# Kernel tuning notes

Measured on AMD Instinct MI355X. Metric: run time of the kernel, lower is better.

## Reference

```python
import jax, jax.numpy as jnp
import numpy as np
import math

K_SLOTS = 64
DIM = 512
HEADS = 8
HEAD_DIM = DIM // HEADS
EPS = 1e-20
LN_EPS = 1e-5
SQRT_DIM = 1.0 / math.sqrt(HEAD_DIM)


def layernorm(x, g, b):
    mu = jnp.mean(x, axis=-1, keepdims=True)
    var = jnp.var(x, axis=-1, keepdims=True)
    return (x - mu) * jax.lax.rsqrt(var + LN_EPS) * g + b


def setup_inputs() -> dict:
    key = jax.random.key(0)
    ks = jax.random.split(key, 8)
    B, T = 8, 8192
    lim = 1.0 / math.sqrt(DIM)
    return {
        "X": jax.random.normal(ks[0], (B, T, DIM), jnp.float32),
        "slots_w": jax.random.normal(ks[1], (K_SLOTS, DIM), jnp.float32),
        "g_slots": jnp.ones((DIM,), jnp.float32),
        "b_slots": jnp.zeros((DIM,), jnp.float32),
        "Wk": jax.random.uniform(ks[2], (DIM, DIM), jnp.float32, -lim, lim),
        "bk": jax.random.uniform(ks[3], (DIM,), jnp.float32, -lim, lim),
        "Wv": jax.random.uniform(ks[4], (DIM, DIM), jnp.float32, -lim, lim),
        "bv": jax.random.uniform(ks[5], (DIM,), jnp.float32, -lim, lim),
        "g_after": jnp.ones((DIM,), jnp.float32),
        "b_after": jnp.zeros((DIM,), jnp.float32),
    }


def reference(X, slots_w, g_slots, b_slots, Wk, bk, Wv, bv, g_after, b_after):
    B, T, D = X.shape
    # slots -> queries, shared across batch: (K, D) -> (H, K, hd)
    S = layernorm(slots_w, g_slots, b_slots)
    Q = S.reshape(K_SLOTS, HEADS, HEAD_DIM).transpose(1, 0, 2)  # (H, K, hd)
    # key/value projections, head split: (B, T, D) -> (B, H, T, hd)
    Kx = (X @ Wk.T + bk).reshape(B, T, HEADS, HEAD_DIM).transpose(0, 2, 1, 3)
    V = (X @ Wv.T + bv).reshape(B, T, HEADS, HEAD_DIM).transpose(0, 2, 1, 3)
    # attention logits (B, H, K, T), scale = 1/sqrt(head_dim)
    A = jnp.einsum("hkd,bhsd->bhks", Q, Kx) * SQRT_DIM
    # softmax over the SLOT axis (k), then renormalize by row-sum over s
    W = jax.nn.softmax(A, axis=-2)
    C = jnp.sum(W, axis=-1, keepdims=True)  # (B, H, K, 1)
    A = W / (C + EPS)
    S_hat = jnp.einsum("bhks,bhsd->bhkd", A, V)  # (B, H, K, hd)
    S_hat = S_hat.transpose(0, 2, 1, 3).reshape(B, K_SLOTS, D)
    return layernorm(S_hat, g_after, b_after)
```

## Files before the change

kernel.cpp:

```cpp
#include <hip/hip_runtime.h>
#include <hip/hip_bf16.h>
#include <math.h>

typedef unsigned short ushort_t;
typedef unsigned int u32;

constexpr int D  = 512;
constexpr int T  = 8192;
constexpr int B  = 8;
constexpr int H  = 8;
constexpr int KS = 64;
constexpr int HD = 64;
constexpr float SCALE = 0.125f;
constexpr float LNEPS = 1e-5f;
constexpr float EPS   = 1e-20f;

constexpr int TC  = 128;
constexpr int CPB = 2;

constexpr size_t OFF_S    = 0;
constexpr size_t OFF_BQ   = 32768;
constexpr size_t OFF_SACC = 33280;
constexpr size_t OFF_CACC = 295424;
constexpr size_t OFF_WB2  = 299520;

typedef __attribute__((ext_vector_type(8))) short bf16x8;
typedef __attribute__((ext_vector_type(4))) float f32x4;
typedef __attribute__((ext_vector_type(4))) unsigned short us4;

typedef const __attribute__((address_space(1))) u32* gas_ptr;
typedef __attribute__((address_space(3))) u32* las_ptr;

__device__ __forceinline__ void gload16(const void* g, void* l) {
  __builtin_amdgcn_global_load_lds((gas_ptr)g, (las_ptr)l, 16, 0, 0);
}

__device__ __forceinline__ ushort_t f2bf(float x) {
  __hip_bfloat16 t = __float2bfloat16(x);
  return *(ushort_t*)&t;
}

__device__ __forceinline__ u32 pk2bf(float x, float y) {
  __hip_bfloat162 t = __float22bfloat162_rn(make_float2(x, y));
  return *(u32*)&t;
}

__device__ __forceinline__ bf16x8 cvt8(f32x4 a, f32x4 b) {
  union { bf16x8 v; u32 u[4]; } r;
  r.u[0] = pk2bf(a.x, a.y); r.u[1] = pk2bf(a.z, a.w);
  r.u[2] = pk2bf(b.x, b.y); r.u[3] = pk2bf(b.z, b.w);
  return r.v;
}

__global__ void ln_slots_kernel(const float* __restrict__ slots_w,
                                const float* __restrict__ g, const float* __restrict__ b,
                                float* __restrict__ S) {
  __shared__ float red[8];
  int k = blockIdx.x;
  int tid = threadIdx.x;
  float x0 = slots_w[k*D + tid];
  float x1 = slots_w[k*D + tid + 256];
  float s1 = x0 + x1, s2 = x0*x0 + x1*x1;
  for (int off = 32; off; off >>= 1) { s1 += __shfl_xor(s1, off); s2 += __shfl_xor(s2, off); }
  if ((tid & 63) == 0) { red[tid >> 6] = s1; red[4 + (tid >> 6)] = s2; }
  __syncthreads();
  s1 = red[0] + red[1] + red[2] + red[3];
  s2 = red[4] + red[5] + red[6] + red[7];
  float mu = s1 / D;
  float var = s2 / D - mu * mu;
  float rs = rsqrtf(var + LNEPS);
  S[k*D + tid]       = (x0 - mu) * rs * g[tid]       + b[tid];
  S[k*D + tid + 256] = (x1 - mu) * rs * g[tid + 256] + b[tid + 256];
}

__global__ void weff_kernel(const float* __restrict__ S, const float* __restrict__ Wk,
                            ushort_t* __restrict__ Wb2) {
  int gid = blockIdx.x * 256 + threadIdx.x;
  int in = gid & 511;
  int hk = gid >> 9;
  int h = hk >> 6, k = hk & 63;
  const float* srow = S + k*D + h*HD;
  const float* wcol = Wk + (size_t)(h*HD)*D + in;
  float acc = 0.f;
  #pragma unroll 8
  for (int d = 0; d < HD; ++d) acc += srow[d] * wcol[(size_t)d*D];
  Wb2[(size_t)(h*128 + k)*D + in] = f2bf(acc * SCALE);
}

__global__ void bq_kernel(const float* __restrict__ S, const float* __restrict__ bk,
                          float* __restrict__ bq) {
  int hk = blockIdx.x * 256 + threadIdx.x;
  int h = hk >> 6, k = hk & 63;
  float acc = 0.f;
  for (int d = 0; d < HD; ++d) acc += S[k*D + h*HD + d] * bk[h*HD + d];
  bq[hk] = acc * SCALE;
}

__global__ void wvcopy_kernel(const float* __restrict__ Wv, ushort_t* __restrict__ Wb2) {
  int gid = blockIdx.x * 256 + threadIdx.x;
  int in = gid & 511;
  int hd = gid >> 9;
  int h = hd >> 6, d = hd & 63;
  Wb2[(size_t)(h*128 + 64 + d)*D + in] = f2bf(Wv[(size_t)hd*D + in]);
}

__global__ void zero_kernel(float* __restrict__ p, int n) {
  int gid = blockIdx.x * 256 + threadIdx.x;
  if (gid < n) p[gid] = 0.f;
}

__global__ __launch_bounds__(256, 3) void main_kernel(
    const float* __restrict__ X, const ushort_t* __restrict__ Wb2,
    const float* __restrict__ bq, const float* __restrict__ bv,
    float* __restrict__ Sacc, float* __restrict__ Cacc) {
  __shared__ __align__(16) char smem[34816];
  float*    A_lds = (float*)smem;
  ushort_t* B_lds = (ushort_t*)(smem + 16384);
  ushort_t* W_lds = (ushort_t*)smem;
  ushort_t* V_lds = (ushort_t*)(smem + 17408);

  const int tid  = threadIdx.x;
  const int lane = tid & 63, w = tid >> 6;
  const int wm = w & 1, wn = w >> 1;
  const int m16 = lane & 15, q = lane >> 4;

  const int id = blockIdx.x;
  const int h  = (id >> 3) & 7;
  const int cg = (id & 7) | ((id >> 6) << 3);
  const int bh = (cg >> 5) * H + h;

  f32x4 acc2[4] = {};
  float csum[4] = {0.f, 0.f, 0.f, 0.f};

  for (int cc = 0; cc < CPB; ++cc) {
    const float* Xc = X + (size_t)(cg * CPB + cc) * TC * D;
    f32x4 acc[4][4] = {};

    for (int kb = 0; kb < D; kb += 32) {
      __syncthreads();
      #pragma unroll
      for (int m = 0; m < 4; ++m) {
        int li = tid + m * 256;
        int row = li >> 3, c = li & 7;
        gload16(Xc + (size_t)row * D + kb + c * 4, A_lds + (size_t)li * 4);
      }
      #pragma unroll
      for (int m = 0; m < 2; ++m) {
        int li = tid + m * 256;
        int col = li >> 2, c = li & 3;
        gload16(Wb2 + (size_t)(h * 128 + col) * D + kb + c * 8, B_lds + (size_t)li * 8);
      }
      __syncthreads();
      bf16x8 af[4], bf[4];
      #pragma unroll
      for (int i = 0; i < 4; ++i) {
        const f32x4* ap = (const f32x4*)(A_lds + (wm * 64 + i * 16 + m16) * 32 + q * 8);
        af[i] = cvt8(ap[0], ap[1]);
      }
      #pragma unroll
      for (int j = 0; j < 4; ++j)
        bf[j] = *(const bf16x8*)(B_lds + (wn * 64 + j * 16 + m16) * 32 + q * 8);
      #pragma unroll
      for (int i = 0; i < 4; ++i)
        #pragma unroll
        for (int j = 0; j < 4; ++j)
          acc[i][j] = __builtin_amdgcn_mfma_f32_16x16x32_bf16(af[i], bf[j], acc[i][j], 0, 0, 0);
    }
    __syncthreads();

    if (wn == 0) {
      float bqv[4];
      #pragma unroll
      for (int j = 0; j < 4; ++j) bqv[j] = bq[h * KS + j * 16 + m16];
      #pragma unroll
      for (int i = 0; i < 4; ++i) {
        us4 wp[4];
        #pragma unroll
        for (int r = 0; r < 4; ++r) {
          float v0 = acc[i][0][r] + bqv[0];
          float v1 = acc[i][1][r] + bqv[1];
          float v2 = acc[i][2][r] + bqv[2];
          float v3 = acc[i][3][r] + bqv[3];
          float mx = fmaxf(fmaxf(v0, v1), fmaxf(v2, v3));
          mx = fmaxf(mx, __shfl_xor(mx, 1));
          mx = fmaxf(mx, __shfl_xor(mx, 2));
          mx = fmaxf(mx, __shfl_xor(mx, 4));
          mx = fmaxf(mx, __shfl_xor(mx, 8));
          v0 = __expf(v0 - mx); v1 = __expf(v1 - mx);
          v2 = __expf(v2 - mx); v3 = __expf(v3 - mx);
          float s = v0 + v1 + v2 + v3;
          s += __shfl_xor(s, 1); s += __shfl_xor(s, 2);
          s += __shfl_xor(s, 4); s += __shfl_xor(s, 8);
          float inv = __builtin_amdgcn_rcpf(s);
          v0 *= inv; v1 *= inv; v2 *= inv; v3 *= inv;
          csum[0] += v0; csum[1] += v1; csum[2] += v2; csum[3] += v3;
          wp[0][r] = f2bf(v0); wp[1][r] = f2bf(v1);
          wp[2][r] = f2bf(v2); wp[3][r] = f2bf(v3);
        }
        #pragma unroll
        for (int j = 0; j < 4; ++j)
          *(us4*)(W_lds + (j * 16 + m16) * 136 + wm * 64 + i * 16 + q * 4) = wp[j];
      }
    } else {
      float bvv[4];
      #pragma unroll
      for (int j = 0; j < 4; ++j) bvv[j] = bv[h * HD + j * 16 + m16];
      #pragma unroll
      for (int i = 0; i < 4; ++i) {
        #pragma unroll
        for (int j = 0; j < 4; ++j) {
          us4 pk;
          pk.x = f2bf(acc[i][j][0] + bvv[j]);
          pk.y = f2bf(acc[i][j][1] + bvv[j]);
          pk.z = f2bf(acc[i][j][2] + bvv[j]);
          pk.w = f2bf(acc[i][j][3] + bvv[j]);
          *(us4*)(V_lds + (j * 16 + m16) * 136 + wm * 64 + i * 16 + q * 4) = pk;
        }
      }
    }
    __syncthreads();

    #pragma unroll
    for (int kk = 0; kk < 4; ++kk) {
      bf16x8 a = *(const bf16x8*)(W_lds + (w * 16 + m16) * 136 + kk * 32 + q * 8);
      #pragma unroll
      for (int j = 0; j < 4; ++j) {
        bf16x8 bb = *(const bf16x8*)(V_lds + (j * 16 + m16) * 136 + kk * 32 + q * 8);
        acc2[j] = __builtin_amdgcn_mfma_f32_16x16x32_bf16(a, bb, acc2[j], 0, 0, 0);
      }
    }
  }

  float* Sb = Sacc + (size_t)bh * KS * HD;
  #pragma unroll
  for (int j = 0; j < 4; ++j)
    #pragma unroll
    for (int r = 0; r < 4; ++r)
      atomicAdd(Sb + (w * 16 + q * 4 + r) * HD + j * 16 + m16, acc2[j][r]);

  if (wn == 0) {
    #pragma unroll
    for (int j = 0; j < 4; ++j) {
      float c = csum[j];
      c += __shfl_xor(c, 16);
      c += __shfl_xor(c, 32);
      if (q == 0) atomicAdd(Cacc + (size_t)bh * KS + j * 16 + m16, c);
    }
  }
}

__global__ void finalize_kernel(const float* __restrict__ Sacc, const float* __restrict__ Cacc,
                                const float* __restrict__ g, const float* __restrict__ bb,
                                float* __restrict__ out) {
  __shared__ float red[8];
  int bk_ = blockIdx.x;
  int b = bk_ >> 6, k = bk_ & 63;
  int tid = threadIdx.x;
  float v[2];
  #pragma unroll
  for (int m = 0; m < 2; ++m) {
    int d = tid + m*256;
    int h = d >> 6, dd = d & 63;
    float c = Cacc[((size_t)b*H + h)*KS + k];
    v[m] = Sacc[(((size_t)b*H + h)*KS + k)*HD + dd] / (c + EPS);
  }
  float s1 = v[0] + v[1], s2 = v[0]*v[0] + v[1]*v[1];
  for (int off = 32; off; off >>= 1) { s1 += __shfl_xor(s1, off); s2 += __shfl_xor(s2, off); }
  if ((tid & 63) == 0) { red[tid >> 6] = s1; red[4 + (tid >> 6)] = s2; }
  __syncthreads();
  s1 = red[0] + red[1] + red[2] + red[3];
  s2 = red[4] + red[5] + red[6] + red[7];
  float mu = s1 / D;
  float var = s2 / D - mu * mu;
  float rs = rsqrtf(var + LNEPS);
  #pragma unroll
  for (int m = 0; m < 2; ++m) {
    int d = tid + m*256;
    out[(size_t)bk_*D + d] = (v[m] - mu) * rs * g[d] + bb[d];
  }
}

extern "C" void kernel_launch(void* const* d_in, const int* in_sizes, int n_in,
                              void* d_out, int out_size, void* d_ws, size_t ws_size,
                              hipStream_t stream) {
  const float* X       = (const float*)d_in[0];
  const float* slots_w = (const float*)d_in[1];
  const float* g_slots = (const float*)d_in[2];
  const float* b_slots = (const float*)d_in[3];
  const float* Wk      = (const float*)d_in[4];
  const float* bk      = (const float*)d_in[5];
  const float* Wv      = (const float*)d_in[6];
  const float* bv      = (const float*)d_in[7];
  const float* g_after = (const float*)d_in[8];
  const float* b_after = (const float*)d_in[9];
  float* ws   = (float*)d_ws;
  float* S    = ws + OFF_S;
  float* bq   = ws + OFF_BQ;
  float* Sacc = ws + OFF_SACC;
  float* Cacc = ws + OFF_CACC;
  ushort_t* Wb2 = (ushort_t*)(ws + OFF_WB2);
  float* out  = (float*)d_out;

  hipLaunchKernelGGL(ln_slots_kernel, dim3(64), dim3(256), 0, stream, slots_w, g_slots, b_slots, S);
  hipLaunchKernelGGL(weff_kernel, dim3(1024), dim3(256), 0, stream, S, Wk, Wb2);
  hipLaunchKernelGGL(bq_kernel, dim3(2), dim3(256), 0, stream, S, bk, bq);
  hipLaunchKernelGGL(wvcopy_kernel, dim3(1024), dim3(256), 0, stream, Wv, Wb2);
  hipLaunchKernelGGL(zero_kernel, dim3(1040), dim3(256), 0, stream, Sacc, 266240);
  hipLaunchKernelGGL(main_kernel, dim3(2048), dim3(256), 0, stream, X, Wb2, bq, bv, Sacc, Cacc);
  hipLaunchKernelGGL(finalize_kernel, dim3(B * KS), dim3(256), 0, stream,
                     Sacc, Cacc, g_after, b_after, out);
}
```

Before: 363.0 us.

## Pre-convert X to bf16 and run swizzled-LDS bf16 main kernel

```diff
diff --git a/kernel.cpp b/kernel.cpp
--- a/kernel.cpp
+++ b/kernel.cpp
@@ -23,6 +23,8 @@
 constexpr size_t OFF_SACC = 33280;
 constexpr size_t OFF_CACC = 295424;
 constexpr size_t OFF_WB2  = 299520;
+constexpr size_t OFF_XB   = 561664;
+constexpr size_t WS_NEED  = (OFF_XB + (size_t)B*T*D/2) * 4;
 
 typedef __attribute__((ext_vector_type(8))) short bf16x8;
 typedef __attribute__((ext_vector_type(4))) float f32x4;
@@ -109,13 +111,20 @@
   if (gid < n) p[gid] = 0.f;
 }
 
-__global__ __launch_bounds__(256, 3) void main_kernel(
-    const float* __restrict__ X, const ushort_t* __restrict__ Wb2,
+__global__ void xcvt_kernel(const float* __restrict__ X, ushort_t* __restrict__ Xb) {
+  size_t i = ((size_t)blockIdx.x * 256 + threadIdx.x) * 8;
+  f32x4 a = *(const f32x4*)(X + i);
+  f32x4 b = *(const f32x4*)(X + i + 4);
+  *(bf16x8*)(Xb + i) = cvt8(a, b);
+}
+
+__global__ __launch_bounds__(256, 4) void main_kernel_bf16(
+    const ushort_t* __restrict__ Xb, const ushort_t* __restrict__ Wb2,
     const float* __restrict__ bq, const float* __restrict__ bv,
     float* __restrict__ Sacc, float* __restrict__ Cacc) {
   __shared__ __align__(16) char smem[34816];
-  float*    A_lds = (float*)smem;
-  ushort_t* B_lds = (ushort_t*)(smem + 16384);
+  ushort_t* A_lds = (ushort_t*)smem;
+  ushort_t* B_lds = (ushort_t*)(smem + 8192);
   ushort_t* W_lds = (ushort_t*)smem;
   ushort_t* V_lds = (ushort_t*)(smem + 17408);
 
@@ -123,6 +132,7 @@
   const int lane = tid & 63, w = tid >> 6;
   const int wm = w & 1, wn = w >> 1;
   const int m16 = lane & 15, q = lane >> 4;
+  const int kq = q ^ ((m16 >> 1) & 3);
 
   const int id = blockIdx.x;
   const int h  = (id >> 3) & 7;
@@ -133,38 +143,38 @@
   float csum[4] = {0.f, 0.f, 0.f, 0.f};
 
   for (int cc = 0; cc < CPB; ++cc) {
-    const float* Xc = X + (size_t)(cg * CPB + cc) * TC * D;
+    const ushort_t* Xc = Xb + (size_t)(cg * CPB + cc) * TC * D;
     f32x4 acc[4][4] = {};
 
     for (int kb = 0; kb < D; kb += 32) {
       __syncthreads();
       #pragma unroll
-      for (int m = 0; m < 4; ++m) {
-        int li = tid + m * 256;
-        int row = li >> 3, c = li & 7;
-        gload16(Xc + (size_t)row * D + kb + c * 4, A_lds + (size_t)li * 4);
-      }
-      #pragma unroll
       for (int m = 0; m < 2; ++m) {
         int li = tid + m * 256;
-        int col = li >> 2, c = li & 3;
-        gload16(Wb2 + (size_t)(h * 128 + col) * D + kb + c * 8, B_lds + (size_t)li * 8);
+        int row = li >> 2;
+        int kc = (li & 3) ^ ((row >> 1) & 3);
+        gload16(Xc + (size_t)row * D + kb + kc * 8, A_lds + (size_t)li * 8);
+      }
+      #pragma unroll
+      for (int m = 0; m < 2; ++m) {
+        int li = tid + m * 256;
+        int col = li >> 2;
+        int kc = (li & 3) ^ ((col >> 1) & 3);
+        gload16(Wb2 + (size_t)(h * 128 + col) * D + kb + kc * 8, B_lds + (size_t)li * 8);
       }
       __syncthreads();
-      bf16x8 af[4], bf[4];
-      #pragma unroll
-      for (int i = 0; i < 4; ++i) {
-        const f32x4* ap = (const f32x4*)(A_lds + (wm * 64 + i * 16 + m16) * 32 + q * 8);
-        af[i] = cvt8(ap[0], ap[1]);
-      }
+      bf16x8 af[4], bfv[4];
+      #pragma unroll
+      for (int i = 0; i < 4; ++i)
+        af[i] = *(const bf16x8*)(A_lds + (size_t)(((wm*64 + i*16 + m16) << 2) | kq) * 8);
       #pragma unroll
       for (int j = 0; j < 4; ++j)
-        bf[j] = *(const bf16x8*)(B_lds + (wn * 64 + j * 16 + m16) * 32 + q * 8);
+        bfv[j] = *(const bf16x8*)(B_lds + (size_t)(((wn*64 + j*16 + m16) << 2) | kq) * 8);
       #pragma unroll
       for (int i = 0; i < 4; ++i)
         #pragma unroll
         for (int j = 0; j < 4; ++j)
-          acc[i][j] = __builtin_amdgcn_mfma_f32_16x16x32_bf16(af[i], bf[j], acc[i][j], 0, 0, 0);
+          acc[i][j] = __builtin_amdgcn_mfma_f32_16x16x32_bf16(af[i], bfv[j], acc[i][j], 0, 0, 0);
     }
     __syncthreads();
 
@@ -249,6 +259,145 @@
   }
 }
 
+__global__ __launch_bounds__(256, 3) void main_kernel_f32(
+    const float* __restrict__ X, const ushort_t* __restrict__ Wb2,
+    const float* __restrict__ bq, const float* __restrict__ bv,
+    float* __restrict__ Sacc, float* __restrict__ Cacc) {
+  __shared__ __align__(16) char smem[34816];
+  float*    A_lds = (float*)smem;
+  ushort_t* B_lds = (ushort_t*)(smem + 16384);
+  ushort_t* W_lds = (ushort_t*)smem;
+  ushort_t* V_lds = (ushort_t*)(smem + 17408);
+
+  const int tid  = threadIdx.x;
+  const int lane = tid & 63, w = tid >> 6;
+  const int wm = w & 1, wn = w >> 1;
+  const int m16 = lane & 15, q = lane >> 4;
+
+  const int id = blockIdx.x;
+  const int h  = (id >> 3) & 7;
+  const int cg = (id & 7) | ((id >> 6) << 3);
+  const int bh = (cg >> 5) * H + h;
+
+  f32x4 acc2[4] = {};
+  float csum[4] = {0.f, 0.f, 0.f, 0.f};
+
+  for (int cc = 0; cc < CPB; ++cc) {
+    const float* Xc = X + (size_t)(cg * CPB + cc) * TC * D;
+    f32x4 acc[4][4] = {};
+    for (int kb = 0; kb < D; kb += 32) {
+      __syncthreads();
+      #pragma unroll
+      for (int m = 0; m < 4; ++m) {
+        int li = tid + m * 256;
+        int row = li >> 3, c = li & 7;
+        gload16(Xc + (size_t)row * D + kb + c * 4, A_lds + (size_t)li * 4);
+      }
+      #pragma unroll
+      for (int m = 0; m < 2; ++m) {
+        int li = tid + m * 256;
+        int col = li >> 2, c = li & 3;
+        gload16(Wb2 + (size_t)(h * 128 + col) * D + kb + c * 8, B_lds + (size_t)li * 8);
+      }
+      __syncthreads();
+      bf16x8 af[4], bfv[4];
+      #pragma unroll
+      for (int i = 0; i < 4; ++i) {
+        const f32x4* ap = (const f32x4*)(A_lds + (wm * 64 + i * 16 + m16) * 32 + q * 8);
+        af[i] = cvt8(ap[0], ap[1]);
+      }
+      #pragma unroll
+      for (int j = 0; j < 4; ++j)
+        bfv[j] = *(const bf16x8*)(B_lds + (wn * 64 + j * 16 + m16) * 32 + q * 8);
+      #pragma unroll
+      for (int i = 0; i < 4; ++i)
+        #pragma unroll
+        for (int j = 0; j < 4; ++j)
+          acc[i][j] = __builtin_amdgcn_mfma_f32_16x16x32_bf16(af[i], bfv[j], acc[i][j], 0, 0, 0);
+    }
+    __syncthreads();
+
+    if (wn == 0) {
+      float bqv[4];
+      #pragma unroll
+      for (int j = 0; j < 4; ++j) bqv[j] = bq[h * KS + j * 16 + m16];
+      #pragma unroll
+      for (int i = 0; i < 4; ++i) {
+        us4 wp[4];
+        #pragma unroll
+        for (int r = 0; r < 4; ++r) {
+          float v0 = acc[i][0][r] + bqv[0];
+          float v1 = acc[i][1][r] + bqv[1];
+          float v2 = acc[i][2][r] + bqv[2];
+          float v3 = acc[i][3][r] + bqv[3];
+          float mx = fmaxf(fmaxf(v0, v1), fmaxf(v2, v3));
+          mx = fmaxf(mx, __shfl_xor(mx, 1));
+          mx = fmaxf(mx, __shfl_xor(mx, 2));
+          mx = fmaxf(mx, __shfl_xor(mx, 4));
+          mx = fmaxf(mx, __shfl_xor(mx, 8));
+          v0 = __expf(v0 - mx); v1 = __expf(v1 - mx);
+          v2 = __expf(v2 - mx); v3 = __expf(v3 - mx);
+          float s = v0 + v1 + v2 + v3;
+          s += __shfl_xor(s, 1); s += __shfl_xor(s, 2);
+          s += __shfl_xor(s, 4); s += __shfl_xor(s, 8);
+          float inv = __builtin_amdgcn_rcpf(s);
+          v0 *= inv; v1 *= inv; v2 *= inv; v3 *= inv;
+          csum[0] += v0; csum[1] += v1; csum[2] += v2; csum[3] += v3;
+          wp[0][r] = f2bf(v0); wp[1][r] = f2bf(v1);
+          wp[2][r] = f2bf(v2); wp[3][r] = f2bf(v3);
+        }
+        #pragma unroll
+        for (int j = 0; j < 4; ++j)
+          *(us4*)(W_lds + (j * 16 + m16) * 136 + wm * 64 + i * 16 + q * 4) = wp[j];
+      }
+    } else {
+      float bvv[4];
+      #pragma unroll
+      for (int j = 0; j < 4; ++j) bvv[j] = bv[h * HD + j * 16 + m16];
+      #pragma unroll
+      for (int i = 0; i < 4; ++i) {
+        #pragma unroll
+        for (int j = 0; j < 4; ++j) {
+          us4 pk;
+          pk.x = f2bf(acc[i][j][0] + bvv[j]);
+          pk.y = f2bf(acc[i][j][1] + bvv[j]);
+          pk.z = f2bf(acc[i][j][2] + bvv[j]);
+          pk.w = f2bf(acc[i][j][3] + bvv[j]);
+          *(us4*)(V_lds + (j * 16 + m16) * 136 + wm * 64 + i * 16 + q * 4) = pk;
+        }
+      }
+    }
+    __syncthreads();
+
+    #pragma unroll
+    for (int kk = 0; kk < 4; ++kk) {
+      bf16x8 a = *(const bf16x8*)(W_lds + (w * 16 + m16) * 136 + kk * 32 + q * 8);
+      #pragma unroll
+      for (int j = 0; j < 4; ++j) {
+        bf16x8 bb = *(const bf16x8*)(V_lds + (j * 16 + m16) * 136 + kk * 32 + q * 8);
+        acc2[j] = __builtin_amdgcn_mfma_f32_16x16x32_bf16(a, bb, acc2[j], 0, 0, 0);
+      }
+    }
+  }
+
+  float* Sb = Sacc + (size_t)bh * KS * HD;
+  #pragma unroll
+  for (int j = 0; j < 4; ++j)
+    #pragma unroll
+    for (int r = 0; r < 4; ++r)
+      atomicAdd(Sb + (w * 16 + q * 4 + r) * HD + j * 16 + m16, acc2[j][r]);
+
+  if (wn == 0) {
+    #pragma unroll
+    for (int j = 0; j < 4; ++j) {
+      float c = csum[j];
+      c += __shfl_xor(c, 16);
+      c += __shfl_xor(c, 32);
+      if (q == 0) atomicAdd(Cacc + (size_t)bh * KS + j * 16 + m16, c);
+    }
+  }
+}
+
 __global__ void finalize_kernel(const float* __restrict__ Sacc, const float* __restrict__ Cacc,
                                 const float* __restrict__ g, const float* __restrict__ bb,
                                 float* __restrict__ out) {
@@ -299,6 +448,7 @@
   float* Sacc = ws + OFF_SACC;
   float* Cacc = ws + OFF_CACC;
   ushort_t* Wb2 = (ushort_t*)(ws + OFF_WB2);
+  ushort_t* Xb  = (ushort_t*)(ws + OFF_XB);
   float* out  = (float*)d_out;
 
   hipLaunchKernelGGL(ln_slots_kernel, dim3(64), dim3(256), 0, stream, slots_w, g_slots, b_slots, S);
@@ -306,7 +456,14 @@
   hipLaunchKernelGGL(bq_kernel, dim3(2), dim3(256), 0, stream, S, bk, bq);
   hipLaunchKernelGGL(wvcopy_kernel, dim3(1024), dim3(256), 0, stream, Wv, Wb2);
   hipLaunchKernelGGL(zero_kernel, dim3(1040), dim3(256), 0, stream, Sacc, 266240);
-  hipLaunchKernelGGL(main_kernel, dim3(2048), dim3(256), 0, stream, X, Wb2, bq, bv, Sacc, Cacc);
+  if (ws_size >= WS_NEED) {
+    hipLaunchKernelGGL(xcvt_kernel, dim3(16384), dim3(256), 0, stream, X, Xb);
+    hipLaunchKernelGGL(main_kernel_bf16, dim3(2048), dim3(256), 0, stream,
+                       Xb, Wb2, bq, bv, Sacc, Cacc);
+  } else {
+    hipLaunchKernelGGL(main_kernel_f32, dim3(2048), dim3(256), 0, stream,
+                       X, Wb2, bq, bv, Sacc, Cacc);
+  }
   hipLaunchKernelGGL(finalize_kernel, dim3(B * KS), dim3(256), 0, stream,
                      Sacc, Cacc, g_after, b_after, out);
 }
```

Result: slower. 416.5 us (+14.7%).
